# Kernel tuning notes

Measured on AMD Instinct MI355X. Metric: run time of the kernel, lower is better.

Reference implementation:

```python
import jax, jax.numpy as jnp
import numpy as np

B, INP, OUP = 16, 64, 64
T, H, W = 30, 64, 44
KD, KH, KW = 3, 3, 3
M, G = 2, 2
INP_GAP = max(16, INP // 16)          # 16
GROUPS = G * OUP                       # 128 (wn_fc2 groups)
IN_PG = (M * OUP) // GROUPS            # 1  in-channels per group
OUT_PG = (OUP * INP * KD * KH * KW) // GROUPS  # 864 out-channels per group


def setup_inputs() -> dict:
    key = jax.random.key(0)
    ks = jax.random.split(key, 6)
    x = jax.random.normal(ks[0], (B, INP, T, H, W), dtype=jnp.float32)
    # reduce: 1x1x1 conv INP -> INP_GAP (with bias), acts on [B, INP, 1,1,1]
    w_reduce = jax.random.normal(ks[1], (INP_GAP, INP), dtype=jnp.float32) * 0.05
    b_reduce = jax.random.normal(ks[2], (INP_GAP,), dtype=jnp.float32) * 0.05
    # wn_fc1: 1x1x1 conv INP_GAP -> M*OUP (with bias)
    w_fc1 = jax.random.normal(ks[3], (M * OUP, INP_GAP), dtype=jnp.float32) * 0.05
    b_fc1 = jax.random.normal(ks[4], (M * OUP,), dtype=jnp.float32) * 0.05
    # wn_fc2: grouped 1x1x1 conv, no bias: [groups, out_per_group, in_per_group]
    w_fc2 = jax.random.normal(ks[5], (GROUPS, OUT_PG, IN_PG), dtype=jnp.float32) * 0.02
    return {"x": x, "w_reduce": w_reduce, "b_reduce": b_reduce,
            "w_fc1": w_fc1, "b_fc1": b_fc1, "w_fc2": w_fc2}


def reference(x, w_reduce, b_reduce, w_fc1, b_fc1, w_fc2):
    # Global average pool over T,H,W -> [B, INP]; 1x1x1 convs are matmuls.
    x_gap = x.mean(axis=(2, 3, 4))                       # [B, INP]
    g = x_gap @ w_reduce.T + b_reduce                     # [B, INP_GAP]
    h = jax.nn.sigmoid(g @ w_fc1.T + b_fc1)               # [B, M*OUP]
    # Grouped 1x1 conv (groups=GROUPS): group-major channel layout matches
    # torch's conv output ordering, so a plain reshape reproduces .view().
    hg = h.reshape(B, GROUPS, IN_PG)                      # [B, G*OUP, 1]
    wdyn = jnp.einsum('goi,bgi->bgo', w_fc2, hg)          # [B, GROUPS, OUT_PG]
    wdyn = wdyn.reshape(B, OUP, INP, KD, KH, KW)          # per-sample conv weights

    # Per-sample conv3d (groups=1), stride 1, padding 1 on D,H,W.
    def conv_one(xi, wi):
        # xi: [INP, T, H, W], wi: [OUP, INP, KD, KH, KW]
        return jax.lax.conv_general_dilated(
            xi[None], wi, window_strides=(1, 1, 1),
            padding=[(1, 1), (1, 1), (1, 1)],
            dimension_numbers=('NCDHW', 'OIDHW', 'NCDHW'))[0]

    return jax.vmap(conv_one)(x, wdyn)                    # [B, OUP, T, H, W]
```

## Files before the change

### kernel.cpp

```cpp
#include <hip/hip_runtime.h>
#include <hip/hip_bf16.h>
#include <stdint.h>

#define B_ 16
#define T_ 30
#define H_ 64
#define W_ 44
#define HW_ (H_*W_)
#define THW_ (T_*HW_)

#define HP_ 66
#define WP_ 46
#define PPLANE_ (HP_*WP_)
#define PPOS_ (T_*PPLANE_)

#define NS 1080

#define SWZ(v) (((v) >> 1) & 3)

typedef __bf16 bf16x8 __attribute__((ext_vector_type(8)));
typedef float f32x4 __attribute__((ext_vector_type(4)));

static __device__ __forceinline__ short f2bf(float f) {
    __hip_bfloat16 h = __float2bfloat16(f);
    union { __hip_bfloat16 b; short s; } u; u.b = h; return u.s;
}

static __device__ __forceinline__ void gload_lds16(const short* g, short* l) {
    __builtin_amdgcn_global_load_lds((const __attribute__((address_space(1))) void*)g,
                                     (__attribute__((address_space(3))) void*)l, 16, 0, 0);
}

__global__ __launch_bounds__(256) void transpose_kernel(const float* __restrict__ x,
                                                        short* __restrict__ xt,
                                                        float* __restrict__ gap) {
    __shared__ short lb[64*52];
    __shared__ float gsum[64];
    int blk = blockIdx.x;
    int b = blk / (T_*HP_);
    int r = blk - b*(T_*HP_);
    int t = r / HP_;
    int hp = r - t*HP_;
    int tid = threadIdx.x;
    bool interior = (hp >= 1) && (hp <= H_);
    float rsum = 0.f;
    {
        int ic = tid >> 2, g = tid & 3;
        if (interior) {
            int h = hp - 1;
            const float4* row = (const float4*)(x + ((size_t)(b*64 + ic)*T_ + t)*HW_ + h*W_);
            #pragma unroll
            for (int q = g; q < 11; q += 4) {
                float4 v = row[q];
                short4 s4;
                s4.x = f2bf(v.x); s4.y = f2bf(v.y); s4.z = f2bf(v.z); s4.w = f2bf(v.w);
                *(short4*)&lb[ic*52 + q*4] = s4;
                rsum += (v.x + v.y) + (v.z + v.w);
            }
        }
        rsum += __shfl_xor(rsum, 1);
        rsum += __shfl_xor(rsum, 2);
        if ((tid & 3) == 0) gsum[ic] = rsum;
    }
    __syncthreads();
    if (interior && tid < 64)
        atomicAdd(&gap[b*64 + tid], gsum[tid] * (1.0f / THW_));
    for (int e = tid; e < WP_*16; e += 256) {
        int wp = e >> 4, i4 = (e & 15) * 4;
        short4 s4 = make_short4(0,0,0,0);
        if (interior && wp >= 1 && wp <= W_) {
            int w = wp - 1;
            s4.x = lb[(i4+0)*52 + w];
            s4.y = lb[(i4+1)*52 + w];
            s4.z = lb[(i4+2)*52 + w];
            s4.w = lb[(i4+3)*52 + w];
        }
        size_t pos = (size_t)t*PPLANE_ + hp*WP_ + wp;
        short* dst = xt + ((size_t)(b*2 + (i4 >> 5))*PPOS_ + pos)*32 + (i4 & 31);
        *(short4*)dst = s4;
    }
}

__global__ __launch_bounds__(256) void fc_kernel(const float* __restrict__ gap,
        const float* __restrict__ w_reduce, const float* __restrict__ b_reduce,
        const float* __restrict__ w_fc1, const float* __restrict__ b_fc1,
        float* __restrict__ h_out) {
    __shared__ float gl[256];
    int t = threadIdx.x;
    {
        int b = t >> 4, j = t & 15;
        float a = b_reduce[j];
        #pragma unroll
        for (int c = 0; c < 64; ++c) a += gap[b*64 + c] * w_reduce[j*64 + c];
        gl[b*16 + j] = a;
    }
    __syncthreads();
    for (int idx = t; idx < 2048; idx += 256) {
        int b = idx >> 7, j = idx & 127;
        float v = b_fc1[j];
        #pragma unroll
        for (int i = 0; i < 16; ++i) v += gl[b*16 + i] * w_fc1[j*16 + i];
        h_out[idx] = 1.0f / (1.0f + expf(-v));
    }
}

__global__ __launch_bounds__(256) void wdyn_kernel(const float* __restrict__ w_fc2,
        const float* __restrict__ h, short* __restrict__ wdyn, short* __restrict__ zblk) {
    if (blockIdx.x == 0 && threadIdx.x < 128) zblk[threadIdx.x] = 0;
    int b = blockIdx.x / 27, tap = blockIdx.x % 27;
    short* dst = wdyn + ((size_t)b*27 + tap) * 4096;
    for (int e = threadIdx.x; e < 4096; e += 256) {
        int oc = e >> 6, ic = e & 63;
        float wv = w_fc2[(oc*64 + ic)*27 + tap];
        float hv = h[b*128 + 2*oc + (ic >> 5)];
        dst[e] = f2bf(wv * hv);
    }
}

#define MF4(J, BV) do {                                                \
    acc[0][J] = __builtin_amdgcn_mfma_f32_16x16x32_bf16(a0, BV, acc[0][J], 0, 0, 0); \
    acc[1][J] = __builtin_amdgcn_mfma_f32_16x16x32_bf16(a1, BV, acc[1][J], 0, 0, 0); \
    acc[2][J] = __builtin_amdgcn_mfma_f32_16x16x32_bf16(a2, BV, acc[2][J], 0, 0, 0); \
    acc[3][J] = __builtin_amdgcn_mfma_f32_16x16x32_bf16(a3, BV, acc[3][J], 0, 0, 0); \
} while (0)

#define MFMA32(B0,B1,B2,B3,B4,B5,B6,B7) do {                           \
    __builtin_amdgcn_s_setprio(1);                                     \
    MF4(0,B0); MF4(1,B1); MF4(2,B2); MF4(3,B3);                        \
    MF4(4,B4); MF4(5,B5); MF4(6,B6); MF4(7,B7);                        \
    __builtin_amdgcn_s_setprio(0);                                     \
} while (0)

#define AREAD() do {                                                   \
    int _cw = (kg ^ SWZ(ln)) * 8;                                      \
    a0 = *(const bf16x8*)&wb[(ln     )*32 + _cw];                      \
    a1 = *(const bf16x8*)&wb[(ln + 16)*32 + _cw];                      \
    a2 = *(const bf16x8*)&wb[(ln + 32)*32 + _cw];                      \
    a3 = *(const bf16x8*)&wb[(ln + 48)*32 + _cw];                      \
} while (0)

#define BROW(Y, DST) do {                                              \
    int _s = sbase + (Y)*18;                                           \
    DST = *(const bf16x8*)&xs[_s*32 + ((kg ^ SWZ(_s)) * 8)];           \
} while (0)

#define PUBLISH() do {                                                 \
    __syncthreads();                                                   \
    *(uint4*)wdst = wr;                                                \
    __syncthreads();                                                   \
} while (0)

__global__ __launch_bounds__(256, 2) void conv_kernel(const short* __restrict__ xt,
        const short* __restrict__ wdyn, const short* __restrict__ zblk,
        float* __restrict__ out) {
    __shared__ short xs[NS*32 + 256];
    __shared__ short wb[2048];

    int bid = (blockIdx.x & 7) * 384 + (blockIdx.x >> 3);
    int b = bid / 192; int r = bid - b*192;
    int tzt = r / 24; r -= tzt*24;
    int tyt = r / 3;  int txt = r - tyt*3;
    int t0 = tzt*4, h0 = tyt*8, w0 = txt*16;

    int tid = threadIdx.x, wid = tid >> 6, lane = tid & 63;
    int ln = lane & 15, kg = lane >> 4;
    int l4 = lane >> 2, c = lane & 3;
    int tzw = wid;
    int woc = tid >> 2, wseg = tid & 3;

    const short* wdb   = wdyn + (size_t)b * 27 * 4096;
    const short* wbase = wdb + woc*64 + wseg*8;
    short* wdst = wb + woc*32 + ((wseg ^ SWZ(woc)) * 8);

    f32x4 acc[4][8];
    #pragma unroll
    for (int mt = 0; mt < 4; ++mt)
        #pragma unroll
        for (int j = 0; j < 8; ++j) acc[mt][j] = f32x4{0.f, 0.f, 0.f, 0.f};

    auto stage_x = [&](int half) {
        const short* xbh = xt + (size_t)(b*2 + half) * PPOS_ * 32;
        #pragma unroll 2
        for (int ii = 0; ii < 17; ++ii) {
            int inst = wid*17 + ii;
            int s = inst*16 + l4;
            int z = s / 180; int rr2 = s - z*180;
            int y = rr2 / 18; int xx = rr2 - y*18;
            int t = t0 + z - 1;
            int seg = (c ^ SWZ(s)) * 8;
            const short* src = ((unsigned)t < (unsigned)T_)
                ? xbh + ((size_t)t*PPLANE_ + (h0+y)*WP_ + (w0+xx))*32 + seg
                : zblk + seg;
            gload_lds16(src, xs + inst*512);
        }
    };

    stage_x(0);
    uint4 wr = *(const uint4*)(wbase);

    int kd = 0, kw = 0, hoff = 0;
    bf16x8 a0, a1, a2, a3;
    bf16x8 r0, r1, r2, r3, r4, r5, r6, r7, r8, r9;

    #pragma unroll 1
    for (int ss = 0; ss < 18; ++ss) {
        int nkw  = (kw == 2) ? 0 : kw + 1;
        int nkd  = (kw == 2) ? ((kd == 2) ? 0 : kd + 1) : kd;
        int nhoff = (kw == 2 && kd == 2) ? 32 : hoff;
        int sbase = (tzw + kd)*180 + kw + ln;
        int tb = kd*9 + kw;

        PUBLISH();
        wr = *(const uint4*)(wbase + (tb + 3)*4096 + hoff);
        BROW(0, r0); BROW(1, r1); BROW(2, r2); BROW(3, r3); BROW(4, r4);
        BROW(5, r5); BROW(6, r6); BROW(7, r7); BROW(8, r8); BROW(9, r9);
        AREAD();
        MFMA32(r0, r1, r2, r3, r4, r5, r6, r7);
        PUBLISH();
        wr = *(const uint4*)(wbase + (tb + 6)*4096 + hoff);
        AREAD();
        MFMA32(r1, r2, r3, r4, r5, r6, r7, r8);
        PUBLISH();
        if (ss < 17)
            wr = *(const uint4*)(wbase + (nkd*9 + nkw)*4096 + nhoff);
        AREAD();
        MFMA32(r2, r3, r4, r5, r6, r7, r8, r9);

        if (ss == 8) {
            __syncthreads();
            stage_x(1);
            asm volatile("s_waitcnt vmcnt(0)" ::: "memory");
            __builtin_amdgcn_s_barrier();
        }
        kd = nkd; kw = nkw; hoff = nhoff;
    }

    int t = t0 + tzw;
    int wv = w0 + ln;
    if (t < T_ && wv < W_) {
        #pragma unroll
        for (int mt = 0; mt < 4; ++mt) {
            size_t obase = ((size_t)(b*64 + mt*16 + kg*4) * T_ + t) * HW_;
            #pragma unroll
            for (int j = 0; j < 8; ++j) {
                float* o = out + obase + (h0 + j)*W_ + wv;
                #pragma unroll
                for (int ri = 0; ri < 4; ++ri)
                    o[(size_t)ri * THW_] = acc[mt][j][ri];
            }
        }
    }
}

extern "C" void kernel_launch(void* const* d_in, const int* in_sizes, int n_in,
                              void* d_out, int out_size, void* d_ws, size_t ws_size,
                              hipStream_t stream) {
    const float* x        = (const float*)d_in[0];
    const float* w_reduce = (const float*)d_in[1];
    const float* b_reduce = (const float*)d_in[2];
    const float* w_fc1    = (const float*)d_in[3];
    const float* b_fc1    = (const float*)d_in[4];
    const float* w_fc2    = (const float*)d_in[5];
    float* out = (float*)d_out;

    float* gap  = (float*)d_ws;
    float* h    = gap + 1024;
    short* wdyn = (short*)(h + 2048);
    short* zblk = wdyn + (size_t)B_*27*4096;
    short* xt   = zblk + 128;

    hipMemsetAsync(gap, 0, 1024*sizeof(float), stream);
    transpose_kernel<<<B_*T_*HP_, 256, 0, stream>>>(x, xt, gap);
    fc_kernel       <<<1,         256, 0, stream>>>(gap, w_reduce, b_reduce, w_fc1, b_fc1, h);
    wdyn_kernel     <<<B_*27,     256, 0, stream>>>(w_fc2, h, wdyn, zblk);
    conv_kernel     <<<B_*192,    256, 0, stream>>>(xt, wdyn, zblk, out);
}
```

Before: 605.1 us.

## Shrink conv tile to 2 time slices and split rows across waves for occupancy

The conv block tile drops from 4 time slices by 8 rows to 2 slices by 8 rows. The four waves now split as 2 time slices by 2 four-row halves, so each wave holds half as many accumulators and fewer B-row registers. This cuts LDS use and registers, allowing 3 blocks per CU, and the padded T dimension no longer wastes work (30 divides by 2). The cost is more halo overhead, since 4 z-planes are staged for 2 output planes instead of 6 for 4. Each block also loads its dynamic weights separately, and blocks now twice as many, which raises total weight and input traffic.

```diff
diff --git a/kernel.cpp b/kernel.cpp
--- a/kernel.cpp
+++ b/kernel.cpp
@@ -14,7 +14,7 @@
 #define PPLANE_ (HP_*WP_)
 #define PPOS_ (T_*PPLANE_)
 
-#define NS 1080
+#define NS2 720
 
 #define SWZ(v) (((v) >> 1) & 3)
 
@@ -124,10 +124,9 @@
     acc[3][J] = __builtin_amdgcn_mfma_f32_16x16x32_bf16(a3, BV, acc[3][J], 0, 0, 0); \
 } while (0)
 
-#define MFMA32(B0,B1,B2,B3,B4,B5,B6,B7) do {                           \
+#define MFMA16(B0,B1,B2,B3) do {                                       \
     __builtin_amdgcn_s_setprio(1);                                     \
     MF4(0,B0); MF4(1,B1); MF4(2,B2); MF4(3,B3);                        \
-    MF4(4,B4); MF4(5,B5); MF4(6,B6); MF4(7,B7);                        \
     __builtin_amdgcn_s_setprio(0);                                     \
 } while (0)
 
@@ -139,8 +138,8 @@
     a3 = *(const bf16x8*)&wb[(ln + 48)*32 + _cw];                      \
 } while (0)
 
-#define BROW(Y, DST) do {                                              \
-    int _s = sbase + (Y)*18;                                           \
+#define BROW(M, DST) do {                                              \
+    int _s = sbro + (M)*18;                                            \
     DST = *(const bf16x8*)&xs[_s*32 + ((kg ^ SWZ(_s)) * 8)];           \
 } while (0)
 
@@ -150,81 +149,90 @@
     __syncthreads();                                                   \
 } while (0)
 
-__global__ __launch_bounds__(256, 2) void conv_kernel(const short* __restrict__ xt,
+__global__ __launch_bounds__(256, 3) void conv_kernel(const short* __restrict__ xt,
         const short* __restrict__ wdyn, const short* __restrict__ zblk,
         float* __restrict__ out) {
-    __shared__ short xs[NS*32 + 256];
+    __shared__ short xs[NS2*32];
     __shared__ short wb[2048];
 
-    int bid = (blockIdx.x & 7) * 384 + (blockIdx.x >> 3);
-    int b = bid / 192; int r = bid - b*192;
+    int bid = (blockIdx.x & 7) * 720 + (blockIdx.x >> 3);
+    int b = bid / 360; int r = bid - b*360;
     int tzt = r / 24; r -= tzt*24;
     int tyt = r / 3;  int txt = r - tyt*3;
-    int t0 = tzt*4, h0 = tyt*8, w0 = txt*16;
+    int t0 = tzt*2, h0 = tyt*8, w0 = txt*16;
 
     int tid = threadIdx.x, wid = tid >> 6, lane = tid & 63;
     int ln = lane & 15, kg = lane >> 4;
     int l4 = lane >> 2, c = lane & 3;
-    int tzw = wid;
+    int tzw = wid & 1, hw4 = (wid >> 1) * 4;
     int woc = tid >> 2, wseg = tid & 3;
 
     const short* wdb   = wdyn + (size_t)b * 27 * 4096;
     const short* wbase = wdb + woc*64 + wseg*8;
     short* wdst = wb + woc*32 + ((wseg ^ SWZ(woc)) * 8);
 
-    f32x4 acc[4][8];
+    f32x4 acc[4][4];
     #pragma unroll
     for (int mt = 0; mt < 4; ++mt)
         #pragma unroll
-        for (int j = 0; j < 8; ++j) acc[mt][j] = f32x4{0.f, 0.f, 0.f, 0.f};
+        for (int j = 0; j < 4; ++j) acc[mt][j] = f32x4{0.f, 0.f, 0.f, 0.f};
 
     auto stage_x = [&](int half) {
         const short* xbh = xt + (size_t)(b*2 + half) * PPOS_ * 32;
-        #pragma unroll 2
-        for (int ii = 0; ii < 17; ++ii) {
-            int inst = wid*17 + ii;
-            int s = inst*16 + l4;
-            int z = s / 180; int rr2 = s - z*180;
-            int y = rr2 / 18; int xx = rr2 - y*18;
-            int t = t0 + z - 1;
-            int seg = (c ^ SWZ(s)) * 8;
-            const short* src = ((unsigned)t < (unsigned)T_)
-                ? xbh + ((size_t)t*PPLANE_ + (h0+y)*WP_ + (w0+xx))*32 + seg
-                : zblk + seg;
-            gload_lds16(src, xs + inst*512);
+        #pragma unroll
+        for (int ii = 0; ii < 12; ++ii) {
+            int inst = ii*4 + wid;
+            if (inst < 45) {
+                int s = inst*16 + l4;
+                int z = s / 180; int rr = s - z*180;
+                int y = rr / 18; int xx = rr - y*18;
+                int t = t0 + z - 1;
+                int seg = (c ^ SWZ(s)) * 8;
+                const short* src = ((unsigned)t < (unsigned)T_)
+                    ? xbh + ((size_t)t*PPLANE_ + (h0+y)*WP_ + (w0+xx))*32 + seg
+                    : zblk + seg;
+                gload_lds16(src, xs + inst*512);
+            }
         }
     };
 
     stage_x(0);
     uint4 wr = *(const uint4*)(wbase);
-
-    int kd = 0, kw = 0, hoff = 0;
+    asm volatile("s_waitcnt vmcnt(0)" ::: "memory");
+    __builtin_amdgcn_s_barrier();
+
     bf16x8 a0, a1, a2, a3;
-    bf16x8 r0, r1, r2, r3, r4, r5, r6, r7, r8, r9;
+    bf16x8 r0, r1, r2, r3, r4, r5;
 
     #pragma unroll 1
     for (int ss = 0; ss < 18; ++ss) {
-        int nkw  = (kw == 2) ? 0 : kw + 1;
-        int nkd  = (kw == 2) ? ((kd == 2) ? 0 : kd + 1) : kd;
-        int nhoff = (kw == 2 && kd == 2) ? 32 : hoff;
-        int sbase = (tzw + kd)*180 + kw + ln;
+        int kdkw = ss - ((ss >= 9) ? 9 : 0);
+        int kd = kdkw / 3, kw = kdkw - kd*3;
+        int hoff = (ss >= 9) ? 32 : 0;
         int tb = kd*9 + kw;
+        int sbro = (tzw + kd)*180 + hw4*18 + kw + ln;
+
+        BROW(0, r0); BROW(1, r1); BROW(2, r2);
+        BROW(3, r3); BROW(4, r4); BROW(5, r5);
 
         PUBLISH();
         wr = *(const uint4*)(wbase + (tb + 3)*4096 + hoff);
-        BROW(0, r0); BROW(1, r1); BROW(2, r2); BROW(3, r3); BROW(4, r4);
-        BROW(5, r5); BROW(6, r6); BROW(7, r7); BROW(8, r8); BROW(9, r9);
         AREAD();
-        MFMA32(r0, r1, r2, r3, r4, r5, r6, r7);
+        MFMA16(r0, r1, r2, r3);
         PUBLISH();
         wr = *(const uint4*)(wbase + (tb + 6)*4096 + hoff);
         AREAD();
-        MFMA32(r1, r2, r3, r4, r5, r6, r7, r8);
+        MFMA16(r1, r2, r3, r4);
         PUBLISH();
-        if (ss < 17)
+        if (ss < 17) {
+            int nss = ss + 1;
+            int nkdkw = nss - ((nss >= 9) ? 9 : 0);
+            int nkd = nkdkw / 3, nkw = nkdkw - nkd*3;
+            int nhoff = (nss >= 9) ? 32 : 0;
             wr = *(const uint4*)(wbase + (nkd*9 + nkw)*4096 + nhoff);
+        }
         AREAD();
-        MFMA32(r2, r3, r4, r5, r6, r7, r8, r9);
+        MFMA16(r2, r3, r4, r5);
 
         if (ss == 8) {
             __syncthreads();
@@ -232,18 +240,17 @@
             asm volatile("s_waitcnt vmcnt(0)" ::: "memory");
             __builtin_amdgcn_s_barrier();
         }
-        kd = nkd; kw = nkw; hoff = nhoff;
     }
 
     int t = t0 + tzw;
     int wv = w0 + ln;
-    if (t < T_ && wv < W_) {
+    if (wv < W_) {
         #pragma unroll
         for (int mt = 0; mt < 4; ++mt) {
             size_t obase = ((size_t)(b*64 + mt*16 + kg*4) * T_ + t) * HW_;
             #pragma unroll
-            for (int j = 0; j < 8; ++j) {
-                float* o = out + obase + (h0 + j)*W_ + wv;
+            for (int j = 0; j < 4; ++j) {
+                float* o = out + obase + (h0 + hw4 + j)*W_ + wv;
                 #pragma unroll
                 for (int ri = 0; ri < 4; ++ri)
                     o[(size_t)ri * THW_] = acc[mt][j][ri];
@@ -273,5 +280,5 @@
     transpose_kernel<<<B_*T_*HP_, 256, 0, stream>>>(x, xt, gap);
     fc_kernel       <<<1,         256, 0, stream>>>(gap, w_reduce, b_reduce, w_fc1, b_fc1, h);
     wdyn_kernel     <<<B_*27,     256, 0, stream>>>(w_fc2, h, wdyn, zblk);
-    conv_kernel     <<<B_*192,    256, 0, stream>>>(xt, wdyn, zblk, out);
-}
+    conv_kernel     <<<B_*360,    256, 0, stream>>>(xt, wdyn, zblk, out);
+}
```

Measured after the change: 524.9 us. 1.15x faster.
